# Kernel optimization log

Measured on AMD Instinct MI355X. Metric: run time of the kernel, lower is better.

The kernel has to match this reference:

```python
import jax, jax.numpy as jnp
import numpy as np

B, S, HID = 1, 2048, 2048
H, KV, D = 16, 8, 128          # heads, kv heads, head_dim
EPS = 1e-6
THETA_T, THETA_HW = 1000000.0, 10000.0
SCALE = D ** -0.5
NEG = -1e9


def _rms(x, w):
    xf = x.astype(jnp.float32)
    var = jnp.mean(xf * xf, axis=-1, keepdims=True)
    return (w * (xf * jax.lax.rsqrt(var + EPS))).astype(x.dtype)


def _rope_cs(pos, theta, half_dim):
    # Module builds RoPE with head_dim = 2*half_dim then takes every-other freq:
    # exponents arange(0, 2*half_dim, 4) / (2*half_dim)  -> half_dim//2 freqs
    dim2 = 2 * half_dim
    inv_freq = 1.0 / theta ** (jnp.arange(0, dim2, 4, dtype=jnp.float32) / dim2)
    freqs = pos.astype(jnp.float32)[:, None] * inv_freq[None, :]   # [S, half_dim//2]
    emb = jnp.concatenate([freqs, freqs], axis=-1)                 # [S, half_dim]
    return jnp.cos(emb), jnp.sin(emb)


def _rot_half(x):
    d = x.shape[-1] // 2
    return jnp.concatenate([-x[..., d:], x[..., :d]], axis=-1)


def _apply_rope(q, k, cos, sin):
    cos = cos[None, None]  # [1,1,S,dim]
    sin = sin[None, None]
    return q * cos + _rot_half(q) * sin, k * cos + _rot_half(k) * sin


def setup_inputs() -> dict:
    key = jax.random.key(0)
    ks = jax.random.split(key, 10)
    hidden_states = jax.random.normal(ks[0], (B, S, HID), jnp.float32)
    indexes = jax.random.randint(ks[1], (3, S), 0, S)
    causal = jnp.tril(jnp.ones((S, S), bool))
    attention_mask = jnp.where(causal, 0.0, NEG).astype(jnp.float32)[None, None]
    qkv_w = jax.random.normal(ks[2], ((H + 2 * KV) * D, HID), jnp.float32) * 0.02
    qkv_b = jax.random.normal(ks[3], ((H + 2 * KV) * D,), jnp.float32) * 0.02
    o_w = jax.random.normal(ks[4], (HID, H * D), jnp.float32) * 0.02
    o_b = jax.random.normal(ks[5], (HID,), jnp.float32) * 0.02
    q_norm_w = jnp.ones((D // 2,), jnp.float32)
    k_norm_w = jnp.ones((D // 2,), jnp.float32)
    q_norm_hw_w = jnp.ones((D // 2,), jnp.float32)
    k_norm_hw_w = jnp.ones((D // 2,), jnp.float32)
    return dict(hidden_states=hidden_states, indexes=indexes, attention_mask=attention_mask,
                qkv_w=qkv_w, qkv_b=qkv_b, o_w=o_w, o_b=o_b,
                q_norm_w=q_norm_w, k_norm_w=k_norm_w,
                q_norm_hw_w=q_norm_hw_w, k_norm_hw_w=k_norm_hw_w)


def reference(hidden_states, indexes, attention_mask, qkv_w, qkv_b, o_w, o_b,
              q_norm_w, k_norm_w, q_norm_hw_w, k_norm_hw_w):
    b, s, _ = hidden_states.shape
    qkv = hidden_states @ qkv_w.T + qkv_b
    q, k, v = jnp.split(qkv, [H * D, H * D + KV * D], axis=-1)
    q = q.reshape(b, s, H, D)
    k = k.reshape(b, s, KV, D)
    v = v.reshape(b, s, KV, D)

    # split head_dim into time half and hw half
    q_t, q_hw = jnp.split(q, 2, axis=-1)
    k_t, k_hw = jnp.split(k, 2, axis=-1)
    q_t = jnp.swapaxes(_rms(q_t, q_norm_w), 1, 2)       # [B,H,S,D/2]
    k_t = jnp.swapaxes(_rms(k_t, k_norm_w), 1, 2)
    q_hw = jnp.swapaxes(_rms(q_hw, q_norm_hw_w), 1, 2)
    k_hw = jnp.swapaxes(_rms(k_hw, k_norm_hw_w), 1, 2)
    q_h, q_ww = jnp.split(q_hw, 2, axis=-1)             # [B,H,S,D/4]
    k_h, k_ww = jnp.split(k_hw, 2, axis=-1)

    cos_t, sin_t = _rope_cs(indexes[0], THETA_T, D // 2)
    q_t, k_t = _apply_rope(q_t, k_t, cos_t, sin_t)
    cos_h, sin_h = _rope_cs(indexes[1], THETA_HW, D // 4)
    q_h, k_h = _apply_rope(q_h, k_h, cos_h, sin_h)
    cos_w, sin_w = _rope_cs(indexes[2], THETA_HW, D // 4)
    q_ww, k_ww = _apply_rope(q_ww, k_ww, cos_w, sin_w)

    query = jnp.concatenate([q_t, q_h, q_ww], axis=-1)  # [B,H,S,D]
    keyst = jnp.concatenate([k_t, k_h, k_ww], axis=-1)  # [B,KV,S,D]
    value = jnp.swapaxes(v, 1, 2)                       # [B,KV,S,D]

    n_rep = H // KV
    keyst = jnp.repeat(keyst, n_rep, axis=1)
    value = jnp.repeat(value, n_rep, axis=1)

    scores = jnp.einsum('bhsd,bhtd->bhst', query, keyst) * SCALE + attention_mask
    probs = jax.nn.softmax(scores.astype(jnp.float32), axis=-1).astype(query.dtype)
    attn = jnp.einsum('bhst,bhtd->bhsd', probs, value)
    attn = jnp.swapaxes(attn, 1, 2).reshape(b, s, H * D)
    return attn @ o_w.T + o_b
```

## Files before the change

kernel.cpp:

```cpp
#include <hip/hip_runtime.h>

typedef __bf16 bf16;
typedef __bf16 bf16x4 __attribute__((ext_vector_type(4)));
typedef __bf16 bf16x8 __attribute__((ext_vector_type(8)));
typedef float f32x4 __attribute__((ext_vector_type(4)));

#define S_LEN 2048
#define HIDDEN 2048
#define NH 16
#define NKV 8
#define HD 128
#define QKV_N 4096

__device__ __forceinline__ void async_load16(const void* g, void* l) {
  __builtin_amdgcn_global_load_lds((const __attribute__((address_space(1))) unsigned int*)g,
                                   (__attribute__((address_space(3))) unsigned int*)l,
                                   16, 0, 0);
}

template <int C>
__device__ __forceinline__ float dpp_f(float x) {
  return __builtin_bit_cast(float, __builtin_amdgcn_mov_dpp(
      __builtin_bit_cast(int, x), C, 0xF, 0xF, true));
}
__device__ __forceinline__ float rowmax16(float x) {
  x = fmaxf(x, dpp_f<0x128>(x));
  x = fmaxf(x, dpp_f<0x124>(x));
  x = fmaxf(x, dpp_f<0x122>(x));
  x = fmaxf(x, dpp_f<0x121>(x));
  return x;
}
__device__ __forceinline__ float rowsum16(float x) {
  x += dpp_f<0x128>(x);
  x += dpp_f<0x124>(x);
  x += dpp_f<0x122>(x);
  x += dpp_f<0x121>(x);
  return x;
}

__global__ __launch_bounds__(256)
void cvt_f32_bf16(const float* __restrict__ src, bf16* __restrict__ dst, int n) {
  int i = (blockIdx.x * 256 + threadIdx.x) * 4;
  if (i < n) {
    float4 v = *(const float4*)(src + i);
    bf16x4 o = {(bf16)v.x, (bf16)v.y, (bf16)v.z, (bf16)v.w};
    *(bf16x4*)(dst + i) = o;
  }
}

template <int WRITE_BF16>
__global__ __launch_bounds__(256)
void gemm_bt(const bf16* __restrict__ A, const bf16* __restrict__ B,
             const float* __restrict__ bias, void* __restrict__ Cout,
             int M, int N, int K) {
  __shared__ bf16 As[128 * 32];
  __shared__ bf16 Bs[128 * 32];
  const int tid = threadIdx.x;
  const int w = tid >> 6, lane = tid & 63;
  const int quad = lane >> 4, l15 = lane & 15;
  const int wm = w >> 1, wn = w & 1;
  const int m0 = blockIdx.y * 128, n0 = blockIdx.x * 128;

  f32x4 acc[4][4];
#pragma unroll
  for (int i = 0; i < 4; i++)
#pragma unroll
    for (int j = 0; j < 4; j++) acc[i][j] = (f32x4){0.f, 0.f, 0.f, 0.f};

  const int crow = lane >> 2;
  const int ccol = (lane & 3) * 8;

  for (int k0 = 0; k0 < K; k0 += 32) {
    __syncthreads();
#pragma unroll
    for (int q = 0; q < 2; q++) {
      int c = 2 * w + q;
      async_load16(A + (size_t)(m0 + c * 16 + crow) * K + k0 + ccol, (char*)As + c * 1024);
      async_load16(B + (size_t)(n0 + c * 16 + crow) * K + k0 + ccol, (char*)Bs + c * 1024);
    }
    __syncthreads();
    bf16x8 af[4], bfr[4];
#pragma unroll
    for (int i = 0; i < 4; i++)
      af[i] = *(const bf16x8*)(As + (wm * 64 + i * 16 + l15) * 32 + quad * 8);
#pragma unroll
    for (int j = 0; j < 4; j++)
      bfr[j] = *(const bf16x8*)(Bs + (wn * 64 + j * 16 + l15) * 32 + quad * 8);
#pragma unroll
    for (int i = 0; i < 4; i++)
#pragma unroll
      for (int j = 0; j < 4; j++)
        acc[i][j] = __builtin_amdgcn_mfma_f32_16x16x32_bf16(af[i], bfr[j], acc[i][j], 0, 0, 0);
  }

#pragma unroll
  for (int i = 0; i < 4; i++) {
#pragma unroll
    for (int j = 0; j < 4; j++) {
      int col = n0 + wn * 64 + j * 16 + l15;
      float bv = bias[col];
#pragma unroll
      for (int r = 0; r < 4; r++) {
        int row = m0 + wm * 64 + i * 16 + quad * 4 + r;
        float v = acc[i][j][r] + bv;
        if (WRITE_BF16)
          ((bf16*)Cout)[(size_t)row * N + col] = (bf16)v;
        else
          ((float*)Cout)[(size_t)row * N + col] = v;
      }
    }
  }
}

__global__ __launch_bounds__(256)
void gemm_bt64(const bf16* __restrict__ A, const bf16* __restrict__ B,
               const float* __restrict__ bias, float* __restrict__ Cout,
               int M, int N, int K) {
  __shared__ bf16 As[128 * 32];
  __shared__ bf16 Bs[64 * 32];
  const int tid = threadIdx.x;
  const int w = tid >> 6, lane = tid & 63;
  const int quad = lane >> 4, l15 = lane & 15;
  const int m0 = blockIdx.y * 128, n0 = blockIdx.x * 64;

  f32x4 acc[2][4];
#pragma unroll
  for (int i = 0; i < 2; i++)
#pragma unroll
    for (int j = 0; j < 4; j++) acc[i][j] = (f32x4){0.f, 0.f, 0.f, 0.f};

  const int crow = lane >> 2;
  const int ccol = (lane & 3) * 8;

  for (int k0 = 0; k0 < K; k0 += 32) {
    __syncthreads();
#pragma unroll
    for (int q = 0; q < 2; q++) {
      int c = 2 * w + q;
      async_load16(A + (size_t)(m0 + c * 16 + crow) * K + k0 + ccol, (char*)As + c * 1024);
    }
    async_load16(B + (size_t)(n0 + w * 16 + crow) * K + k0 + ccol, (char*)Bs + w * 1024);
    __syncthreads();
    bf16x8 af[2], bfr[4];
#pragma unroll
    for (int i = 0; i < 2; i++)
      af[i] = *(const bf16x8*)(As + (w * 32 + i * 16 + l15) * 32 + quad * 8);
#pragma unroll
    for (int j = 0; j < 4; j++)
      bfr[j] = *(const bf16x8*)(Bs + (j * 16 + l15) * 32 + quad * 8);
#pragma unroll
    for (int i = 0; i < 2; i++)
#pragma unroll
      for (int j = 0; j < 4; j++)
        acc[i][j] = __builtin_amdgcn_mfma_f32_16x16x32_bf16(af[i], bfr[j], acc[i][j], 0, 0, 0);
  }

#pragma unroll
  for (int i = 0; i < 2; i++) {
#pragma unroll
    for (int j = 0; j < 4; j++) {
      int col = n0 + j * 16 + l15;
      float bv = bias[col];
#pragma unroll
      for (int r = 0; r < 4; r++) {
        int row = m0 + w * 32 + i * 16 + quad * 4 + r;
        Cout[(size_t)row * N + col] = acc[i][j][r] + bv;
      }
    }
  }
}

__global__ __launch_bounds__(128)
void normrope(const bf16* __restrict__ qkv, const int* __restrict__ idx,
              const float* __restrict__ qnw, const float* __restrict__ knw,
              const float* __restrict__ qnhw, const float* __restrict__ knhw,
              bf16* __restrict__ Qb, bf16* __restrict__ Kb) {
  const int s = blockIdx.x;
  const int y = blockIdx.y;
  const int d = threadIdx.x;

  const bool isq = (y < 16);
  const int off = isq ? (y * HD + d) : (2048 + (y - 16) * HD + d);
  float x = (float)qkv[(size_t)s * QKV_N + off];

  float ss = x * x;
#pragma unroll
  for (int o = 32; o; o >>= 1) ss += __shfl_xor(ss, o);
  float inv = rsqrtf(ss * (1.f / 64.f) + 1e-6f);
  const float* wt = (d < 64) ? (isq ? qnw : knw) : (isq ? qnhw : knhw);
  float yn = x * inv * wt[d & 63];

  float pos, invf;
  int xorm;
  bool firsthalf;
  if (d < 64) {
    pos = (float)idx[s];
    int i = d & 31;
    invf = exp2f(-(float)i * 0.6228615177913804f);
    xorm = 32;
    firsthalf = (d < 32);
  } else {
    int j = d - 64;
    int region = j >> 5;
    pos = (float)idx[(1 + region) * S_LEN + s];
    int i = j & 15;
    invf = exp2f(-(float)i * 0.8304820237218406f);
    xorm = 16;
    firsthalf = ((j & 31) < 16);
  }
  float ang = pos * invf;
  float si, co;
  sincosf(ang, &si, &co);
  float partner = __shfl_xor(yn, xorm);
  float outv = firsthalf ? (yn * co - partner * si) : (yn * co + partner * si);

  if (isq)
    Qb[((size_t)y * S_LEN + s) * HD + d] = (bf16)(outv * 0.12751745f);
  else
    Kb[((size_t)(y - 16) * S_LEN + s) * HD + d] = (bf16)outv;
}

__global__ __launch_bounds__(256)
void vtrans(const bf16* __restrict__ qkv, bf16* __restrict__ VT) {
  __shared__ bf16 T[64][72];
  const int tid = threadIdx.x;
  const int s0 = blockIdx.x * 64, d0 = blockIdx.y * 64, kv = blockIdx.z;
#pragma unroll
  for (int it = 0; it < 2; it++) {
    int r = (tid >> 3) + it * 32;
    int c = (tid & 7) * 8;
    bf16x8 v = *(const bf16x8*)(qkv + (size_t)(s0 + r) * QKV_N + 3072 + kv * HD + d0 + c);
    *(bf16x8*)(&T[r][c]) = v;
  }
  __syncthreads();
#pragma unroll
  for (int it = 0; it < 2; it++) {
    int r = (tid >> 3) + it * 32;
    int c = (tid & 7) * 8;
    bf16x8 o;
#pragma unroll
    for (int j = 0; j < 8; j++) o[j] = T[c + j][r];
    *(bf16x8*)(VT + ((size_t)kv * HD + d0 + r) * S_LEN + s0 + c) = o;
  }
}

__global__ __launch_bounds__(256)
void attn_fused(const bf16* __restrict__ Qb, const bf16* __restrict__ Kb,
                const bf16* __restrict__ VT, bf16* __restrict__ attnO,
                float* __restrict__ Opart, float* __restrict__ Ml) {
  __shared__ bf16 Kbuf[2][8192];
  __shared__ bf16 Vbuf[8192];
  __shared__ __align__(16) bf16 Ps[4][16][72];
  const int tid = threadIdx.x;
  const int w = tid >> 6, lane = tid & 63;
  const int quad = lane >> 4, l15 = lane & 15;
  const int b = blockIdx.x;
  const int h = b & 15;
  const int cid = b >> 4;
  int g, c;
  if (cid < 32) { g = 16 + (cid >> 1); c = cid & 1; }
  else          { g = cid - 32;        c = 0; }
  const int nT = g + 1;
  const int tBeg = c ? 16 : 0;
  const int tEnd = c ? nT : (nT < 16 ? nT : 16);
  const int qr0 = g * 64 + w * 16;
  const int kv = h >> 1;

  const bf16* Qg = Qb + (size_t)h * S_LEN * HD;
  const bf16* Kg = Kb + (size_t)kv * S_LEN * HD;
  const bf16* Vg = VT + (size_t)kv * HD * S_LEN;

  const bf16* ksrc = Kg + (size_t)(w * 16 + l15) * HD + quad * 8;
  const bf16* vsrc = Vg + (size_t)(2 * w * 16 + l15) * S_LEN + quad * 8;

  bf16x8 aq[4];
#pragma unroll
  for (int kc = 0; kc < 4; kc++)
    aq[kc] = *(const bf16x8*)(Qg + (size_t)(qr0 + l15) * HD + kc * 32 + quad * 8);

  float m2[4], li[4];
  f32x4 Oacc[8];
#pragma unroll
  for (int r = 0; r < 4; r++) { m2[r] = -1e30f; li[r] = 0.f; }
#pragma unroll
  for (int dt = 0; dt < 8; dt++) Oacc[dt] = (f32x4){0.f, 0.f, 0.f, 0.f};

#pragma unroll
  for (int kc = 0; kc < 4; kc++)
    async_load16(ksrc + (size_t)(tBeg << 6) * HD + kc * 32,
                 (char*)Kbuf[tBeg & 1] + (w * 4 + kc) * 1024);

  for (int tt = tBeg; tt < tEnd; ++tt) {
    const int t0 = tt << 6;
    const int cur = tt & 1;
    const bool more = (tt + 1 < tEnd);
    __asm__ __volatile__("s_waitcnt vmcnt(0)" ::: "memory");
    __syncthreads();

#pragma unroll
    for (int e = 0; e < 2; e++)
#pragma unroll
      for (int half = 0; half < 2; half++)
        async_load16(vsrc + (size_t)e * 16 * S_LEN + t0 + half * 32,
                     (char*)Vbuf + (half * 8 + 2 * w + e) * 1024);
    if (more) {
#pragma unroll
      for (int kc = 0; kc < 4; kc++)
        async_load16(ksrc + (size_t)(t0 + 64) * HD + kc * 32,
                     (char*)Kbuf[cur ^ 1] + (w * 4 + kc) * 1024);
    }

    f32x4 sacc[4];
#pragma unroll
    for (int nt = 0; nt < 4; nt++) {
      sacc[nt] = (f32x4){0.f, 0.f, 0.f, 0.f};
#pragma unroll
      for (int kc = 0; kc < 4; kc++) {
        bf16x8 bk = *(const bf16x8*)((const char*)Kbuf[cur] + (nt * 4 + kc) * 1024 + lane * 16);
        sacc[nt] = __builtin_amdgcn_mfma_f32_16x16x32_bf16(aq[kc], bk, sacc[nt], 0, 0, 0);
      }
    }

    const bool full = (t0 + 64 <= qr0);
    float mxv[4];
    bool need = false;
#pragma unroll
    for (int r = 0; r < 4; r++) {
      if (!full) {
        const int mrow = qr0 + quad * 4 + r;
        const int cb = t0 + l15;
        if (cb > mrow) sacc[0][r] = -1e30f;
        if (cb + 16 > mrow) sacc[1][r] = -1e30f;
        if (cb + 32 > mrow) sacc[2][r] = -1e30f;
        if (cb + 48 > mrow) sacc[3][r] = -1e30f;
      }
      mxv[r] = rowmax16(fmaxf(fmaxf(sacc[0][r], sacc[1][r]), fmaxf(sacc[2][r], sacc[3][r])));
      need = need || (mxv[r] > m2[r] + 8.f);
    }
    if (__any(need ? 1 : 0)) {
#pragma unroll
      for (int r = 0; r < 4; r++) {
        float mnew = fmaxf(m2[r], mxv[r]);
        float a = exp2f(m2[r] - mnew);
        li[r] *= a;
#pragma unroll
        for (int dt = 0; dt < 8; dt++) Oacc[dt][r] *= a;
        m2[r] = mnew;
      }
    }
#pragma unroll
    for (int r = 0; r < 4; r++) {
      float p0 = exp2f(sacc[0][r] - m2[r]);
      float p1 = exp2f(sacc[1][r] - m2[r]);
      float p2 = exp2f(sacc[2][r] - m2[r]);
      float p3 = exp2f(sacc[3][r] - m2[r]);
      li[r] += rowsum16((p0 + p1) + (p2 + p3));
      Ps[w][quad * 4 + r][l15] = (bf16)p0;
      Ps[w][quad * 4 + r][16 + l15] = (bf16)p1;
      Ps[w][quad * 4 + r][32 + l15] = (bf16)p2;
      Ps[w][quad * 4 + r][48 + l15] = (bf16)p3;
    }
    __asm__ __volatile__("s_waitcnt lgkmcnt(0)" ::: "memory");
    if (more)
      __asm__ __volatile__("s_waitcnt vmcnt(4)" ::: "memory");
    else
      __asm__ __volatile__("s_waitcnt vmcnt(0)" ::: "memory");

#pragma unroll
    for (int half = 0; half < 2; half++) {
      bf16x8 ap = *(const bf16x8*)(&Ps[w][l15][half * 32 + quad * 8]);
#pragma unroll
      for (int dt = 0; dt < 8; dt++) {
        bf16x8 bv = *(const bf16x8*)((const char*)Vbuf + (half * 8 + dt) * 1024 + lane * 16);
        Oacc[dt] = __builtin_amdgcn_mfma_f32_16x16x32_bf16(ap, bv, Oacc[dt], 0, 0, 0);
      }
    }
  }

  if (cid < 32) {
    float* Op = Opart + (size_t)b * 64 * 128;
    float* mlp = Ml + (size_t)b * 128;
#pragma unroll
    for (int r = 0; r < 4; r++) {
      const int row = w * 16 + quad * 4 + r;
#pragma unroll
      for (int dt = 0; dt < 8; dt++)
        Op[row * 128 + dt * 16 + l15] = Oacc[dt][r];
      if (l15 == 0) {
        mlp[row * 2 + 0] = m2[r];
        mlp[row * 2 + 1] = li[r];
      }
    }
  } else {
#pragma unroll
    for (int r = 0; r < 4; r++) {
      float invl = 1.f / li[r];
      int srow = qr0 + quad * 4 + r;
#pragma unroll
      for (int dt = 0; dt < 8; dt++)
        attnO[(size_t)srow * HIDDEN + h * HD + dt * 16 + l15] = (bf16)(Oacc[dt][r] * invl);
    }
  }
}

__global__ __launch_bounds__(256)
void attn_merge(const float* __restrict__ Opart, const float* __restrict__ Ml,
                bf16* __restrict__ attnO) {
  const int h = blockIdx.x & 15;
  const int g = 16 + (blockIdx.x >> 4);
  const int cid0 = (g - 16) * 2;
  const int bA = cid0 * 16 + h, bB = (cid0 + 1) * 16 + h;
  const float* OA = Opart + (size_t)bA * 64 * 128;
  const float* OB = Opart + (size_t)bB * 64 * 128;
  const float* mlA = Ml + (size_t)bA * 128;
  const float* mlB = Ml + (size_t)bB * 128;
  const int t = threadIdx.x;
#pragma unroll
  for (int it = 0; it < 8; ++it) {
    int e = it * 256 + t;
    int row = e >> 5, d = (e & 31) * 4;
    float mA = mlA[row * 2], lA = mlA[row * 2 + 1];
    float mB = mlB[row * 2], lB = mlB[row * 2 + 1];
    float m = fmaxf(mA, mB);
    float aA = exp2f(mA - m), aB = exp2f(mB - m);
    float inv = 1.f / (lA * aA + lB * aB);
    f32x4 a = *(const f32x4*)(OA + row * 128 + d);
    f32x4 bq = *(const f32x4*)(OB + row * 128 + d);
    int srow = g * 64 + row;
    bf16x4 o;
#pragma unroll
    for (int j = 0; j < 4; j++) o[j] = (bf16)((a[j] * aA + bq[j] * aB) * inv);
    *(bf16x4*)(attnO + (size_t)srow * HIDDEN + h * HD + d) = o;
  }
}

extern "C" void kernel_launch(void* const* d_in, const int* in_sizes, int n_in,
                              void* d_out, int out_size, void* d_ws, size_t ws_size,
                              hipStream_t stream) {
  const float* hidden = (const float*)d_in[0];
  const int* idx = (const int*)d_in[1];
  const float* qkv_w = (const float*)d_in[3];
  const float* qkv_b = (const float*)d_in[4];
  const float* o_w = (const float*)d_in[5];
  const float* o_b = (const float*)d_in[6];
  const float* qnw = (const float*)d_in[7];
  const float* knw = (const float*)d_in[8];
  const float* qnhw = (const float*)d_in[9];
  const float* knhw = (const float*)d_in[10];

  char* ws = (char*)d_ws;
  bf16* hB    = (bf16*)(ws);
  bf16* qwB   = (bf16*)(ws + (8u << 20));
  bf16* qkvB  = (bf16*)(ws + (24u << 20));
  bf16* Qb    = (bf16*)(ws + (40u << 20));
  bf16* Kb    = (bf16*)(ws + (48u << 20));
  bf16* VT    = (bf16*)(ws + (52u << 20));
  bf16* owB   = hB;
  float* Opart = (float*)(ws + (8u << 20));
  bf16* attn  = (bf16*)(ws + (24u << 20));
  float* Ml   = (float*)(ws + (32u << 20));

  cvt_f32_bf16<<<HIDDEN * S_LEN / 1024, 256, 0, stream>>>(hidden, hB, HIDDEN * S_LEN);
  cvt_f32_bf16<<<QKV_N * HIDDEN / 1024, 256, 0, stream>>>(qkv_w, qwB, QKV_N * HIDDEN);

  gemm_bt<1><<<dim3(QKV_N / 128, S_LEN / 128), 256, 0, stream>>>(
      hB, qwB, qkv_b, qkvB, S_LEN, QKV_N, HIDDEN);

  cvt_f32_bf16<<<HIDDEN * HIDDEN / 1024, 256, 0, stream>>>(o_w, owB, HIDDEN * HIDDEN);

  normrope<<<dim3(S_LEN, 24), 128, 0, stream>>>(qkvB, idx, qnw, knw, qnhw, knhw, Qb, Kb);
  vtrans<<<dim3(S_LEN / 64, HD / 64, NKV), 256, 0, stream>>>(qkvB, VT);

  attn_fused<<<768, 256, 0, stream>>>(Qb, Kb, VT, attn, Opart, Ml);
  attn_merge<<<256, 256, 0, stream>>>(Opart, Ml, attn);

  gemm_bt64<<<dim3(HIDDEN / 64, S_LEN / 128), 256, 0, stream>>>(
      attn, owB, o_b, (float*)d_out, S_LEN, HIDDEN, HIDDEN);
}
```

Before: 316.8 us.

## Split attention KV range into 13-tile chunks, load V directly to registers

The causal attention work split changes from a 16-tile boundary with up to 2 chunks to 13-tile chunks with up to 3 chunks per query band, giving 912 more evenly sized blocks plus a 3-way merge kernel. V tiles are loaded straight from global memory into registers instead of through an LDS buffer, which frees shared memory, and launch_bounds is raised to target 3 blocks per SM. The workspace layout is reshuffled to hold larger partial-output slots. This trades extra partial writes, merge work and register pressure for better load balance and occupancy.

```diff
diff --git a/kernel.cpp b/kernel.cpp
--- a/kernel.cpp
+++ b/kernel.cpp
@@ -11,6 +11,8 @@
 #define NKV 8
 #define HD 128
 #define QKV_N 4096
+
+#define PSLOT 33280
 
 __device__ __forceinline__ void async_load16(const void* g, void* l) {
   __builtin_amdgcn_global_load_lds((const __attribute__((address_space(1))) unsigned int*)g,
@@ -244,12 +246,11 @@
   }
 }
 
-__global__ __launch_bounds__(256)
+__global__ __launch_bounds__(256, 3)
 void attn_fused(const bf16* __restrict__ Qb, const bf16* __restrict__ Kb,
                 const bf16* __restrict__ VT, bf16* __restrict__ attnO,
-                float* __restrict__ Opart, float* __restrict__ Ml) {
+                char* __restrict__ Opart) {
   __shared__ bf16 Kbuf[2][8192];
-  __shared__ bf16 Vbuf[8192];
   __shared__ __align__(16) bf16 Ps[4][16][72];
   const int tid = threadIdx.x;
   const int w = tid >> 6, lane = tid & 63;
@@ -258,11 +259,12 @@
   const int h = b & 15;
   const int cid = b >> 4;
   int g, c;
-  if (cid < 32) { g = 16 + (cid >> 1); c = cid & 1; }
-  else          { g = cid - 32;        c = 0; }
+  if (cid < 13)      { g = cid; c = 0; }
+  else if (cid < 39) { int t = cid - 13; g = 13 + (t >> 1); c = t & 1; }
+  else               { int t = cid - 39; g = 26 + t / 3;    c = t % 3; }
   const int nT = g + 1;
-  const int tBeg = c ? 16 : 0;
-  const int tEnd = c ? nT : (nT < 16 ? nT : 16);
+  const int tBeg = c * 13;
+  const int tEnd = (tBeg + 13 < nT) ? (tBeg + 13) : nT;
   const int qr0 = g * 64 + w * 16;
   const int kv = h >> 1;
 
@@ -271,7 +273,7 @@
   const bf16* Vg = VT + (size_t)kv * HD * S_LEN;
 
   const bf16* ksrc = Kg + (size_t)(w * 16 + l15) * HD + quad * 8;
-  const bf16* vsrc = Vg + (size_t)(2 * w * 16 + l15) * S_LEN + quad * 8;
+  const bf16* vsrc = Vg + (size_t)l15 * S_LEN + quad * 8;
 
   bf16x8 aq[4];
 #pragma unroll
@@ -297,12 +299,13 @@
     __asm__ __volatile__("s_waitcnt vmcnt(0)" ::: "memory");
     __syncthreads();
 
-#pragma unroll
-    for (int e = 0; e < 2; e++)
-#pragma unroll
-      for (int half = 0; half < 2; half++)
-        async_load16(vsrc + (size_t)e * 16 * S_LEN + t0 + half * 32,
-                     (char*)Vbuf + (half * 8 + 2 * w + e) * 1024);
+    bf16x8 v0[8], v1[8];
+#pragma unroll
+    for (int dt = 0; dt < 8; dt++)
+      v0[dt] = *(const bf16x8*)(vsrc + (size_t)dt * 16 * S_LEN + t0);
+#pragma unroll
+    for (int dt = 0; dt < 8; dt++)
+      v1[dt] = *(const bf16x8*)(vsrc + (size_t)dt * 16 * S_LEN + t0 + 32);
     if (more) {
 #pragma unroll
       for (int kc = 0; kc < 4; kc++)
@@ -366,20 +369,20 @@
     else
       __asm__ __volatile__("s_waitcnt vmcnt(0)" ::: "memory");
 
-#pragma unroll
-    for (int half = 0; half < 2; half++) {
-      bf16x8 ap = *(const bf16x8*)(&Ps[w][l15][half * 32 + quad * 8]);
-#pragma unroll
-      for (int dt = 0; dt < 8; dt++) {
-        bf16x8 bv = *(const bf16x8*)((const char*)Vbuf + (half * 8 + dt) * 1024 + lane * 16);
-        Oacc[dt] = __builtin_amdgcn_mfma_f32_16x16x32_bf16(ap, bv, Oacc[dt], 0, 0, 0);
-      }
-    }
-  }
-
-  if (cid < 32) {
-    float* Op = Opart + (size_t)b * 64 * 128;
-    float* mlp = Ml + (size_t)b * 128;
+    bf16x8 ap0 = *(const bf16x8*)(&Ps[w][l15][quad * 8]);
+#pragma unroll
+    for (int dt = 0; dt < 8; dt++)
+      Oacc[dt] = __builtin_amdgcn_mfma_f32_16x16x32_bf16(ap0, v0[dt], Oacc[dt], 0, 0, 0);
+    bf16x8 ap1 = *(const bf16x8*)(&Ps[w][l15][32 + quad * 8]);
+#pragma unroll
+    for (int dt = 0; dt < 8; dt++)
+      Oacc[dt] = __builtin_amdgcn_mfma_f32_16x16x32_bf16(ap1, v1[dt], Oacc[dt], 0, 0, 0);
+  }
+
+  if (cid >= 13) {
+    char* slot = Opart + (size_t)((cid - 13) * 16 + h) * PSLOT;
+    float* Op = (float*)slot;
+    float* mlp = (float*)(slot + 32768);
 #pragma unroll
     for (int r = 0; r < 4; r++) {
       const int row = w * 16 + quad * 4 + r;
@@ -404,32 +407,42 @@
 }
 
 __global__ __launch_bounds__(256)
-void attn_merge(const float* __restrict__ Opart, const float* __restrict__ Ml,
-                bf16* __restrict__ attnO) {
+void attn_merge(const char* __restrict__ Opart, bf16* __restrict__ attnO) {
   const int h = blockIdx.x & 15;
-  const int g = 16 + (blockIdx.x >> 4);
-  const int cid0 = (g - 16) * 2;
-  const int bA = cid0 * 16 + h, bB = (cid0 + 1) * 16 + h;
-  const float* OA = Opart + (size_t)bA * 64 * 128;
-  const float* OB = Opart + (size_t)bB * 64 * 128;
-  const float* mlA = Ml + (size_t)bA * 128;
-  const float* mlB = Ml + (size_t)bB * 128;
+  const int bandIdx = blockIdx.x >> 4;
+  const int g = 13 + bandIdx;
+  const int nc = (g < 26) ? 2 : 3;
+  const int cid0 = (g < 26) ? (13 + (g - 13) * 2) : (39 + (g - 26) * 3);
+  const char* s0 = Opart + (size_t)((cid0 - 13) * 16 + h) * PSLOT;
+  const char* s1 = Opart + (size_t)((cid0 - 12) * 16 + h) * PSLOT;
+  const char* s2 = Opart + (size_t)((cid0 - 11) * 16 + h) * PSLOT;
+  const float* O0 = (const float*)s0;
+  const float* O1 = (const float*)s1;
+  const float* O2 = (const float*)s2;
+  const float* ML0 = (const float*)(s0 + 32768);
+  const float* ML1 = (const float*)(s1 + 32768);
+  const float* ML2 = (const float*)(s2 + 32768);
   const int t = threadIdx.x;
 #pragma unroll
   for (int it = 0; it < 8; ++it) {
     int e = it * 256 + t;
     int row = e >> 5, d = (e & 31) * 4;
-    float mA = mlA[row * 2], lA = mlA[row * 2 + 1];
-    float mB = mlB[row * 2], lB = mlB[row * 2 + 1];
-    float m = fmaxf(mA, mB);
-    float aA = exp2f(mA - m), aB = exp2f(mB - m);
-    float inv = 1.f / (lA * aA + lB * aB);
-    f32x4 a = *(const f32x4*)(OA + row * 128 + d);
-    f32x4 bq = *(const f32x4*)(OB + row * 128 + d);
+    float m0 = ML0[row * 2], l0 = ML0[row * 2 + 1];
+    float m1 = ML1[row * 2], l1 = ML1[row * 2 + 1];
+    float m2v = -1e30f, l2v = 0.f;
+    if (nc == 3) { m2v = ML2[row * 2]; l2v = ML2[row * 2 + 1]; }
+    float m = fmaxf(fmaxf(m0, m1), m2v);
+    float a0 = exp2f(m0 - m), a1 = exp2f(m1 - m), a2 = exp2f(m2v - m);
+    float inv = 1.f / (a0 * l0 + a1 * l1 + a2 * l2v);
+    f32x4 x0 = *(const f32x4*)(O0 + row * 128 + d);
+    f32x4 x1 = *(const f32x4*)(O1 + row * 128 + d);
+    f32x4 x2 = (f32x4){0.f, 0.f, 0.f, 0.f};
+    if (nc == 3) x2 = *(const f32x4*)(O2 + row * 128 + d);
     int srow = g * 64 + row;
     bf16x4 o;
 #pragma unroll
-    for (int j = 0; j < 4; j++) o[j] = (bf16)((a[j] * aA + bq[j] * aB) * inv);
+    for (int j = 0; j < 4; j++)
+      o[j] = (bf16)((a0 * x0[j] + a1 * x1[j] + a2 * x2[j]) * inv);
     *(bf16x4*)(attnO + (size_t)srow * HIDDEN + h * HD + d) = o;
   }
 }
@@ -450,15 +463,14 @@
 
   char* ws = (char*)d_ws;
   bf16* hB    = (bf16*)(ws);
-  bf16* qwB   = (bf16*)(ws + (8u << 20));
-  bf16* qkvB  = (bf16*)(ws + (24u << 20));
-  bf16* Qb    = (bf16*)(ws + (40u << 20));
-  bf16* Kb    = (bf16*)(ws + (48u << 20));
-  bf16* VT    = (bf16*)(ws + (52u << 20));
+  bf16* Qb    = (bf16*)(ws + (8u << 20));
+  bf16* Kb    = (bf16*)(ws + (16u << 20));
+  bf16* VT    = (bf16*)(ws + (20u << 20));
+  bf16* qwB   = (bf16*)(ws + (24u << 20));
+  bf16* qkvB  = (bf16*)(ws + (40u << 20));
   bf16* owB   = hB;
-  float* Opart = (float*)(ws + (8u << 20));
   bf16* attn  = (bf16*)(ws + (24u << 20));
-  float* Ml   = (float*)(ws + (32u << 20));
+  char* Opart = ws + (32u << 20);
 
   cvt_f32_bf16<<<HIDDEN * S_LEN / 1024, 256, 0, stream>>>(hidden, hB, HIDDEN * S_LEN);
   cvt_f32_bf16<<<QKV_N * HIDDEN / 1024, 256, 0, stream>>>(qkv_w, qwB, QKV_N * HIDDEN);
@@ -471,8 +483,8 @@
   normrope<<<dim3(S_LEN, 24), 128, 0, stream>>>(qkvB, idx, qnw, knw, qnhw, knhw, Qb, Kb);
   vtrans<<<dim3(S_LEN / 64, HD / 64, NKV), 256, 0, stream>>>(qkvB, VT);
 
-  attn_fused<<<768, 256, 0, stream>>>(Qb, Kb, VT, attn, Opart, Ml);
-  attn_merge<<<256, 256, 0, stream>>>(Opart, Ml, attn);
+  attn_fused<<<912, 256, 0, stream>>>(Qb, Kb, VT, attn, Opart);
+  attn_merge<<<304, 256, 0, stream>>>(Opart, attn);
 
   gemm_bt64<<<dim3(HIDDEN / 64, S_LEN / 128), 256, 0, stream>>>(
       attn, owB, o_b, (float*)d_out, S_LEN, HIDDEN, HIDDEN);
```

New measurement: 371.1 us. 17.1% more time.

## Double-buffer LDS in GEMM and use 128x128 tiles for output projection

Applied to the files above, without the earlier changes.

The main bf16 GEMM now keeps two LDS buffers and issues the async global-to-LDS loads for the next K slice before computing the current one, so loads overlap with MFMA work and one barrier per iteration is removed. The separate 64-wide-N output-projection GEMM is deleted and the output projection reuses the double-buffered 128x128 kernel. This doubles LDS use per block and halves the block count for the output projection (256 blocks), which may reduce occupancy on a large-CU GPU.

```diff
diff --git a/kernel.cpp b/kernel.cpp
--- a/kernel.cpp
+++ b/kernel.cpp
@@ -53,8 +53,8 @@
 void gemm_bt(const bf16* __restrict__ A, const bf16* __restrict__ B,
              const float* __restrict__ bias, void* __restrict__ Cout,
              int M, int N, int K) {
-  __shared__ bf16 As[128 * 32];
-  __shared__ bf16 Bs[128 * 32];
+  __shared__ bf16 As[2][128 * 32];
+  __shared__ bf16 Bs[2][128 * 32];
   const int tid = threadIdx.x;
   const int w = tid >> 6, lane = tid & 63;
   const int quad = lane >> 4, l15 = lane & 15;
@@ -70,27 +70,40 @@
   const int crow = lane >> 2;
   const int ccol = (lane & 3) * 8;
 
+#pragma unroll
+  for (int q = 0; q < 2; q++) {
+    int c = 2 * w + q;
+    async_load16(A + (size_t)(m0 + c * 16 + crow) * K + ccol, (char*)As[0] + c * 1024);
+    async_load16(B + (size_t)(n0 + c * 16 + crow) * K + ccol, (char*)Bs[0] + c * 1024);
+  }
+
+  int cur = 0;
   for (int k0 = 0; k0 < K; k0 += 32) {
+    __asm__ __volatile__("s_waitcnt vmcnt(0)" ::: "memory");
     __syncthreads();
-#pragma unroll
-    for (int q = 0; q < 2; q++) {
-      int c = 2 * w + q;
-      async_load16(A + (size_t)(m0 + c * 16 + crow) * K + k0 + ccol, (char*)As + c * 1024);
-      async_load16(B + (size_t)(n0 + c * 16 + crow) * K + k0 + ccol, (char*)Bs + c * 1024);
-    }
-    __syncthreads();
+    if (k0 + 32 < K) {
+#pragma unroll
+      for (int q = 0; q < 2; q++) {
+        int c = 2 * w + q;
+        async_load16(A + (size_t)(m0 + c * 16 + crow) * K + k0 + 32 + ccol,
+                     (char*)As[cur ^ 1] + c * 1024);
+        async_load16(B + (size_t)(n0 + c * 16 + crow) * K + k0 + 32 + ccol,
+                     (char*)Bs[cur ^ 1] + c * 1024);
+      }
+    }
     bf16x8 af[4], bfr[4];
 #pragma unroll
     for (int i = 0; i < 4; i++)
-      af[i] = *(const bf16x8*)(As + (wm * 64 + i * 16 + l15) * 32 + quad * 8);
+      af[i] = *(const bf16x8*)(As[cur] + (wm * 64 + i * 16 + l15) * 32 + quad * 8);
 #pragma unroll
     for (int j = 0; j < 4; j++)
-      bfr[j] = *(const bf16x8*)(Bs + (wn * 64 + j * 16 + l15) * 32 + quad * 8);
+      bfr[j] = *(const bf16x8*)(Bs[cur] + (wn * 64 + j * 16 + l15) * 32 + quad * 8);
 #pragma unroll
     for (int i = 0; i < 4; i++)
 #pragma unroll
       for (int j = 0; j < 4; j++)
         acc[i][j] = __builtin_amdgcn_mfma_f32_16x16x32_bf16(af[i], bfr[j], acc[i][j], 0, 0, 0);
+    cur ^= 1;
   }
 
 #pragma unroll
@@ -107,64 +120,6 @@
           ((bf16*)Cout)[(size_t)row * N + col] = (bf16)v;
         else
           ((float*)Cout)[(size_t)row * N + col] = v;
-      }
-    }
-  }
-}
-
-__global__ __launch_bounds__(256)
-void gemm_bt64(const bf16* __restrict__ A, const bf16* __restrict__ B,
-               const float* __restrict__ bias, float* __restrict__ Cout,
-               int M, int N, int K) {
-  __shared__ bf16 As[128 * 32];
-  __shared__ bf16 Bs[64 * 32];
-  const int tid = threadIdx.x;
-  const int w = tid >> 6, lane = tid & 63;
-  const int quad = lane >> 4, l15 = lane & 15;
-  const int m0 = blockIdx.y * 128, n0 = blockIdx.x * 64;
-
-  f32x4 acc[2][4];
-#pragma unroll
-  for (int i = 0; i < 2; i++)
-#pragma unroll
-    for (int j = 0; j < 4; j++) acc[i][j] = (f32x4){0.f, 0.f, 0.f, 0.f};
-
-  const int crow = lane >> 2;
-  const int ccol = (lane & 3) * 8;
-
-  for (int k0 = 0; k0 < K; k0 += 32) {
-    __syncthreads();
-#pragma unroll
-    for (int q = 0; q < 2; q++) {
-      int c = 2 * w + q;
-      async_load16(A + (size_t)(m0 + c * 16 + crow) * K + k0 + ccol, (char*)As + c * 1024);
-    }
-    async_load16(B + (size_t)(n0 + w * 16 + crow) * K + k0 + ccol, (char*)Bs + w * 1024);
-    __syncthreads();
-    bf16x8 af[2], bfr[4];
-#pragma unroll
-    for (int i = 0; i < 2; i++)
-      af[i] = *(const bf16x8*)(As + (w * 32 + i * 16 + l15) * 32 + quad * 8);
-#pragma unroll
-    for (int j = 0; j < 4; j++)
-      bfr[j] = *(const bf16x8*)(Bs + (j * 16 + l15) * 32 + quad * 8);
-#pragma unroll
-    for (int i = 0; i < 2; i++)
-#pragma unroll
-      for (int j = 0; j < 4; j++)
-        acc[i][j] = __builtin_amdgcn_mfma_f32_16x16x32_bf16(af[i], bfr[j], acc[i][j], 0, 0, 0);
-  }
-
-#pragma unroll
-  for (int i = 0; i < 2; i++) {
-#pragma unroll
-    for (int j = 0; j < 4; j++) {
-      int col = n0 + j * 16 + l15;
-      float bv = bias[col];
-#pragma unroll
-      for (int r = 0; r < 4; r++) {
-        int row = m0 + w * 32 + i * 16 + quad * 4 + r;
-        Cout[(size_t)row * N + col] = acc[i][j][r] + bv;
       }
     }
   }
@@ -474,6 +429,6 @@
   attn_fused<<<768, 256, 0, stream>>>(Qb, Kb, VT, attn, Opart, Ml);
   attn_merge<<<256, 256, 0, stream>>>(Opart, Ml, attn);
 
-  gemm_bt64<<<dim3(HIDDEN / 64, S_LEN / 128), 256, 0, stream>>>(
+  gemm_bt<0><<<dim3(HIDDEN / 128, S_LEN / 128), 256, 0, stream>>>(
       attn, owB, o_b, (float*)d_out, S_LEN, HIDDEN, HIDDEN);
 }
```

Result: no change. 316.4 us (-0.1%).
